# Optimization experiments

Hardware: AMD Instinct MI355X
Metric: run time of the kernel (lower is better)

## Reference

```python
import jax, jax.numpy as jnp
import numpy as np

B, S, D, H = 2, 2048, 1024, 16
HD = D // H  # 64
SCALE = float(np.sqrt(HD))


def setup_inputs() -> dict:
    key = jax.random.key(0)
    ks = jax.random.split(key, 11)
    def lin(kw, kb, fan_in):
        bound = 1.0 / np.sqrt(fan_in)
        W = jax.random.uniform(kw, (D, D), jnp.float32, -bound, bound)
        b = jax.random.uniform(kb, (D,), jnp.float32, -bound, bound)
        return W, b
    Wq, bq = lin(ks[0], ks[1], D)
    Wk, bk = lin(ks[2], ks[3], D)
    Wv, bv = lin(ks[4], ks[5], D)
    Wo, bo = lin(ks[6], ks[7], D)
    q = jax.random.normal(ks[8], (B, S, D), jnp.float32)
    k = jax.random.normal(ks[9], (B, S, D), jnp.float32)
    v = jax.random.normal(ks[10], (B, S, D), jnp.float32)
    mask = jnp.ones((B, 1, S, S), jnp.int32)
    return {"q": q, "k": k, "v": v, "mask": mask,
            "Wq": Wq, "bq": bq, "Wk": Wk, "bk": bk,
            "Wv": Wv, "bv": bv, "Wo": Wo, "bo": bo}


def reference(q, k, v, mask, Wq, bq, Wk, bk, Wv, bv, Wo, bo):
    # torch Linear: x @ W.T + b
    def proj(x, W, b):
        y = x @ W.T + b                      # [B,S,D]
        return y.reshape(B, -1, H, HD).transpose(0, 2, 1, 3)  # [B,H,S,HD]
    Q = proj(q, Wq, bq)
    K = proj(k, Wk, bk)
    V = proj(v, Wv, bv)
    scores = jnp.einsum('bhqd,bhkd->bhqk', Q, K) / SCALE     # [B,H,S,S]
    scores = jnp.where(mask == 0, -1e9, scores)
    attn = jax.nn.softmax(scores, axis=-1)                   # dropout in eval mode = identity
    out = jnp.einsum('bhqk,bhkd->bhqd', attn, V)             # [B,H,S,HD]
    out = out.transpose(0, 2, 1, 3).reshape(B, -1, D)        # [B,S,D]
    return out @ Wo.T + bo
```

## Files before the change

kernel.cpp:

```cpp
#include <hip/hip_runtime.h>
#include <math.h>

#define BB 2
#define SS 2048
#define DD 1024
#define HH 16
#define HDIM 64
#define KK 1024
#define MM 4096
#define KSPLIT 2

#define QFOLD 0.18033688011112042f

typedef _Float16 f16x2 __attribute__((ext_vector_type(2)));
typedef _Float16 f16x4 __attribute__((ext_vector_type(4)));
typedef _Float16 f16x8 __attribute__((ext_vector_type(8)));
typedef float    f32x4 __attribute__((ext_vector_type(4)));

#define GLL16(gp, lp) __builtin_amdgcn_global_load_lds(                        \
    (const __attribute__((address_space(1))) void*)(gp),                       \
    (__attribute__((address_space(3))) void*)(lp), 16, 0, 0)

static __device__ __forceinline__ float fast_exp2(float x) {
    float r;
    asm("v_exp_f32 %0, %1" : "=v"(r) : "v"(x));
    return r;
}
static __device__ __forceinline__ float fast_log2(float x) {
    float r;
    asm("v_log_f32 %0, %1" : "=v"(r) : "v"(x));
    return r;
}
static __device__ __forceinline__ f16x2 cvt_pk(float a, float b) {
    f16x2 r;
    asm("v_cvt_pkrtz_f16_f32 %0, %1, %2" : "=v"(r) : "v"(a), "v"(b));
    return r;
}

__global__ __launch_bounds__(256) void prep(
    const float* __restrict__ q,  const float* __restrict__ k,
    const float* __restrict__ v,  const float* __restrict__ wq,
    const float* __restrict__ wk, const float* __restrict__ wv,
    const float* __restrict__ wo, const int* __restrict__ mask,
    _Float16* __restrict__ qh,  _Float16* __restrict__ kh,
    _Float16* __restrict__ vh,  _Float16* __restrict__ wqh,
    _Float16* __restrict__ wkh, _Float16* __restrict__ wvh,
    _Float16* __restrict__ woh, unsigned short* __restrict__ bm16)
{
    if (blockIdx.x < 16384u) {
        const unsigned u  = blockIdx.x * 256u + threadIdx.x;
        const unsigned U1 = 1u << 20;
        const unsigned U2 = 1u << 18;
        const float* src; _Float16* dst; unsigned off;
        float sc = 1.0f;
        if (u < 3u * U1) {
            const unsigned t = u >> 20; off = u & (U1 - 1u);
            src = (t == 0) ? q  : (t == 1) ? k  : v;
            dst = (t == 0) ? qh : (t == 1) ? kh : vh;
        } else {
            const unsigned r = u - 3u * U1;
            const unsigned t = r >> 18; off = r & (U2 - 1u);
            src = (t == 0) ? wq  : (t == 1) ? wk  : (t == 2) ? wv  : wo;
            dst = (t == 0) ? wqh : (t == 1) ? wkh : (t == 2) ? wvh : woh;
            if (t == 0) sc = QFOLD;
        }
        const float4 x = ((const float4*)src)[off];
        f16x4 y;
        y[0] = (_Float16)(x.x * sc); y[1] = (_Float16)(x.y * sc);
        y[2] = (_Float16)(x.z * sc); y[3] = (_Float16)(x.w * sc);
        ((f16x4*)dst)[off] = y;
    } else {
        const size_t t = (size_t)(blockIdx.x - 16384u) * 256 + threadIdx.x;
        const int4* p = (const int4*)(mask + t * 16);
        const int4 a = p[0], b = p[1], c = p[2], d = p[3];
        unsigned vv = 0;
        vv |= (a.x != 0) << 0;  vv |= (a.y != 0) << 1;
        vv |= (a.z != 0) << 2;  vv |= (a.w != 0) << 3;
        vv |= (b.x != 0) << 4;  vv |= (b.y != 0) << 5;
        vv |= (b.z != 0) << 6;  vv |= (b.w != 0) << 7;
        vv |= (c.x != 0) << 8;  vv |= (c.y != 0) << 9;
        vv |= (c.z != 0) << 10; vv |= (c.w != 0) << 11;
        vv |= (d.x != 0) << 12; vv |= (d.y != 0) << 13;
        vv |= (d.z != 0) << 14; vv |= (d.w != 0) << 15;
        bm16[t] = (unsigned short)vv;
    }
}

#define GEMM_BODY(X, W)                                                        \
    __shared__ _Float16 As[128 * 32];                                          \
    __shared__ _Float16 Bs[64 * 32];                                           \
    const int tid  = threadIdx.x;                                              \
    const int lane = tid & 63;                                                 \
    const int lr   = lane & 15;                                                \
    const int lg   = lane >> 4;                                                \
    const int wave = tid >> 6;                                                 \
    const int wr   = wave >> 1;                                                \
    const int wc   = wave & 1;                                                 \
    const int m0 = blockIdx.y << 7;                                            \
    const int n0 = blockIdx.x << 6;                                            \
    const char* Xb = (const char*)(X);                                         \
    const char* Wb = (const char*)(W);                                         \
    const int pa0 = tid * 16;                                                  \
    const int pa1 = pa0 + 4096;                                                \
    const int ra0 = pa0 >> 6, ca0 = pa0 & 63;                                  \
    const int ra1 = pa1 >> 6, ca1 = pa1 & 63;                                  \
    const int rb0 = pa0 >> 6, cb0 = pa0 & 63;                                  \
    f32x4 acc[4][2] = {};                                                      \
    for (int k0 = 0; k0 < KK; k0 += 32) {                                      \
        GLL16(Xb + ((size_t)(m0 + ra0) * KK + k0) * 2 + ca0, (char*)As + pa0); \
        GLL16(Xb + ((size_t)(m0 + ra1) * KK + k0) * 2 + ca1, (char*)As + pa1); \
        GLL16(Wb + ((size_t)(n0 + rb0) * KK + k0) * 2 + cb0, (char*)Bs + pa0); \
        __syncthreads();                                                       \
        f16x8 af[4], bf[2];                                                    \
        _Pragma("unroll")                                                      \
        for (int mi = 0; mi < 4; ++mi)                                         \
            af[mi] = *(const f16x8*)((const char*)As +                         \
                       ((wr * 64 + mi * 16 + lr) * 64 + lg * 16));             \
        _Pragma("unroll")                                                      \
        for (int ni = 0; ni < 2; ++ni)                                         \
            bf[ni] = *(const f16x8*)((const char*)Bs +                         \
                       ((wc * 32 + ni * 16 + lr) * 64 + lg * 16));             \
        _Pragma("unroll")                                                      \
        for (int mi = 0; mi < 4; ++mi)                                         \
            _Pragma("unroll")                                                  \
            for (int ni = 0; ni < 2; ++ni)                                     \
                acc[mi][ni] = __builtin_amdgcn_mfma_f32_16x16x32_f16(          \
                    af[mi], bf[ni], acc[mi][ni], 0, 0, 0);                     \
        __syncthreads();                                                       \
    }

__global__ __launch_bounds__(256) void gemm_qkv(
    const _Float16* __restrict__ qx, const _Float16* __restrict__ kx,
    const _Float16* __restrict__ vx,
    const _Float16* __restrict__ wqh, const _Float16* __restrict__ wkh,
    const _Float16* __restrict__ wvh,
    const float* __restrict__ bq, const float* __restrict__ bk,
    const float* __restrict__ bv,
    _Float16* __restrict__ Qh, _Float16* __restrict__ Kh,
    _Float16* __restrict__ Vt)
{
    const int z = blockIdx.z;
    const _Float16* X = (z == 0) ? qx : (z == 1) ? kx : vx;
    const _Float16* W = (z == 0) ? wqh : (z == 1) ? wkh : wvh;
    const float* bias = (z == 0) ? bq : (z == 1) ? bk : bv;
    const float bsc   = (z == 0) ? QFOLD : 1.0f;
    _Float16* Yh      = (z == 0) ? Qh : Kh;

    GEMM_BODY(X, W)

    #pragma unroll
    for (int ni = 0; ni < 2; ++ni) {
        const int n  = n0 + wc * 32 + ni * 16 + lr;
        const float bv_ = bias[n] * bsc;
        #pragma unroll
        for (int mi = 0; mi < 4; ++mi) {
            const int mbase = m0 + wr * 64 + mi * 16 + lg * 4;
            if (z < 2) {
                #pragma unroll
                for (int r = 0; r < 4; ++r) {
                    const int m = mbase + r;
                    const int b_ = m >> 11, s_ = m & (SS - 1);
                    const int h_ = n >> 6,  d_ = n & (HDIM - 1);
                    Yh[(((size_t)(b_ * HH + h_)) * SS + s_) * HDIM + d_] =
                        (_Float16)(acc[mi][ni][r] + bv_);
                }
            } else {
                const int b_ = mbase >> 11, s_ = mbase & (SS - 1);
                const int h_ = n >> 6,      d_ = n & (HDIM - 1);
                f16x4 tv;
                #pragma unroll
                for (int r = 0; r < 4; ++r) tv[r] = (_Float16)(acc[mi][ni][r] + bv_);
                *(f16x4*)(Vt + (((size_t)(b_ * HH + h_)) * HDIM + d_) * SS + s_) = tv;
            }
        }
    }
}

__global__ __launch_bounds__(256) void gemm_out(
    const _Float16* __restrict__ X, const _Float16* __restrict__ W,
    const float* __restrict__ bias, float* __restrict__ Y)
{
    GEMM_BODY(X, W)

    #pragma unroll
    for (int ni = 0; ni < 2; ++ni) {
        const int n  = n0 + wc * 32 + ni * 16 + lr;
        const float bv_ = bias[n];
        #pragma unroll
        for (int mi = 0; mi < 4; ++mi) {
            const int mbase = m0 + wr * 64 + mi * 16 + lg * 4;
            #pragma unroll
            for (int r = 0; r < 4; ++r)
                Y[(size_t)(mbase + r) * DD + n] = acc[mi][ni][r] + bv_;
        }
    }
}

__global__ __launch_bounds__(256) void attn_mfma5(
    const _Float16* __restrict__ Qh, const _Float16* __restrict__ Kh,
    const _Float16* __restrict__ Vt, const unsigned long long* __restrict__ bm,
    _Float16* __restrict__ Opart, float* __restrict__ Lpart)
{
    __shared__ _Float16 KbufS[2][4096];
    __shared__ _Float16 VbufS[2][4096];

    const int tid  = threadIdx.x;
    const int lane = tid & 63;
    const int wq   = tid >> 6;
    const int bh   = blockIdx.x;
    const int b_   = bh >> 4;
    const int q0   = blockIdx.y << 7;
    const int ks   = blockIdx.z;
    const int lr   = lane & 15;
    const int lg   = lane >> 4;

    const int NT = SS / 64 / KSPLIT;
    const int t0 = ks * NT;

    const int qrowA = q0 + wq * 32 + lr;
    const int qrowB = qrowA + 16;
    const _Float16* qbA = Qh + ((size_t)bh * SS + qrowA) * HDIM;
    const _Float16* qbB = Qh + ((size_t)bh * SS + qrowB) * HDIM;
    const f16x8 qfA0 = *(const f16x8*)(qbA + lg * 8);
    const f16x8 qfA1 = *(const f16x8*)(qbA + 32 + lg * 8);
    const f16x8 qfB0 = *(const f16x8*)(qbB + lg * 8);
    const f16x8 qfB1 = *(const f16x8*)(qbB + 32 + lg * 8);

    const int c0 = tid, c1 = tid + 256;
    const int kr0 = c0 >> 3, krc0 = (c0 & 7) ^ (kr0 & 7);
    const int kr1 = c1 >> 3, krc1 = (c1 & 7) ^ (kr1 & 7);
    const _Float16* gK0 = Kh + ((size_t)bh * SS + kr0) * HDIM + krc0 * 8;
    const _Float16* gK1 = Kh + ((size_t)bh * SS + kr1) * HDIM + krc1 * 8;
    const _Float16* gV0 = Vt + ((size_t)bh * HDIM + kr0) * SS + krc0 * 8;
    const _Float16* gV1 = Vt + ((size_t)bh * HDIM + kr1) * SS + krc1 * 8;
    const int woff = (tid >> 6) << 10;

    float mA = -INFINITY, mB = -INFINITY;
    f32x4 oaccA[4], oaccB[4];
    #pragma unroll
    for (int dc = 0; dc < 4; ++dc) {
        oaccA[dc] = (f32x4){0.f, 0.f, 0.f, 0.f};
        oaccB[dc] = (f32x4){0.f, 0.f, 0.f, 0.f};
    }
    f32x4 laccA = (f32x4){0.f, 0.f, 0.f, 0.f};
    f32x4 laccB = (f32x4){0.f, 0.f, 0.f, 0.f};

    f16x8 ones;
    #pragma unroll
    for (int e = 0; e < 8; ++e) ones[e] = (_Float16)1.0f;

    const unsigned long long* bmrowA = bm + ((size_t)b_ * SS + qrowA) * (SS / 64);
    const unsigned long long* bmrowB = bm + ((size_t)b_ * SS + qrowB) * (SS / 64);

#define STAGE(KT, BSEL) do {                                                   \
    GLL16(gK0 + (size_t)(KT) * HDIM, (char*)KbufS[BSEL] + woff);               \
    GLL16(gK1 + (size_t)(KT) * HDIM, (char*)KbufS[BSEL] + 4096 + woff);        \
    GLL16(gV0 + (KT), (char*)VbufS[BSEL] + woff);                              \
    GLL16(gV1 + (KT), (char*)VbufS[BSEL] + 4096 + woff);                       \
  } while (0)

    STAGE(t0 * 64, 0);
    __syncthreads();

    const int xk0 = ((lg       ^ (lr & 7)) << 4);
    const int xk1 = (((4 + lg) ^ (lr & 7)) << 4);
    const int xv  = ((lr & 7) << 4);

    unsigned long long bmA = bmrowA[t0];
    unsigned long long bmB = bmrowB[t0];

    for (int ti = 0; ti < NT; ++ti) {
        const int t = t0 + ti;
        const int cur = ti & 1;
        if (ti < NT - 1) STAGE((t + 1) * 64, cur ^ 1);
        unsigned long long bmA_n = 0, bmB_n = 0;
        if (ti < NT - 1) { bmA_n = bmrowA[t + 1]; bmB_n = bmrowB[t + 1]; }

        const char* kb = (const char*)KbufS[cur];
        const char* vb = (const char*)VbufS[cur];

        f32x4 sA[4], sB[4];
        __builtin_amdgcn_s_setprio(1);
        #pragma unroll
        for (int kg = 0; kg < 4; ++kg) {
            const char* rp = kb + (kg * 16 + lr) * 128;
            const f16x8 kf0 = *(const f16x8*)(rp + xk0);
            const f16x8 kf1 = *(const f16x8*)(rp + xk1);
            f32x4 a = (f32x4){0.f, 0.f, 0.f, 0.f};
            a = __builtin_amdgcn_mfma_f32_16x16x32_f16(kf0, qfA0, a, 0, 0, 0);
            a = __builtin_amdgcn_mfma_f32_16x16x32_f16(kf1, qfA1, a, 0, 0, 0);
            sA[kg] = a;
            f32x4 b2 = (f32x4){0.f, 0.f, 0.f, 0.f};
            b2 = __builtin_amdgcn_mfma_f32_16x16x32_f16(kf0, qfB0, b2, 0, 0, 0);
            b2 = __builtin_amdgcn_mfma_f32_16x16x32_f16(kf1, qfB1, b2, 0, 0, 0);
            sB[kg] = b2;
        }
        __builtin_amdgcn_s_setprio(0);

        float svA[16], svB[16];
        #pragma unroll
        for (int kg = 0; kg < 4; ++kg)
            #pragma unroll
            for (int r = 0; r < 4; ++r) {
                svA[kg * 4 + r] = sA[kg][r];
                svB[kg * 4 + r] = sB[kg][r];
            }

        if (~bmA) {
            #pragma unroll
            for (int kg = 0; kg < 4; ++kg)
                #pragma unroll
                for (int r = 0; r < 4; ++r)
                    if (!((bmA >> (kg * 16 + lg * 4 + r)) & 1ull))
                        svA[kg * 4 + r] = -1e9f;
        }
        if (~bmB) {
            #pragma unroll
            for (int kg = 0; kg < 4; ++kg)
                #pragma unroll
                for (int r = 0; r < 4; ++r)
                    if (!((bmB >> (kg * 16 + lg * 4 + r)) & 1ull))
                        svB[kg * 4 + r] = -1e9f;
        }
        bmA = bmA_n; bmB = bmB_n;

        float pmA = svA[0], pmB = svB[0];
        #pragma unroll
        for (int i = 1; i < 16; ++i) {
            pmA = fmaxf(pmA, svA[i]);
            pmB = fmaxf(pmB, svB[i]);
        }
        pmA = fmaxf(pmA, __shfl_xor(pmA, 16));
        pmA = fmaxf(pmA, __shfl_xor(pmA, 32));
        pmB = fmaxf(pmB, __shfl_xor(pmB, 16));
        pmB = fmaxf(pmB, __shfl_xor(pmB, 32));

        if (!__all(pmA <= mA + 8.0f)) {
            const float m_new = fmaxf(mA, pmA);
            const float corr  = fast_exp2(mA - m_new);
            #pragma unroll
            for (int dc = 0; dc < 4; ++dc) oaccA[dc] *= corr;
            laccA *= corr;
            mA = m_new;
        }
        if (!__all(pmB <= mB + 8.0f)) {
            const float m_new = fmaxf(mB, pmB);
            const float corr  = fast_exp2(mB - m_new);
            #pragma unroll
            for (int dc = 0; dc < 4; ++dc) oaccB[dc] *= corr;
            laccB *= corr;
            mB = m_new;
        }

        float pA[16], pB[16];
        #pragma unroll
        for (int i = 0; i < 16; ++i) {
            pA[i] = fast_exp2(svA[i] - mA);
            pB[i] = fast_exp2(svB[i] - mB);
        }

        union { f16x2 h2[4]; f16x8 v8; } uA0, uA1, uB0, uB1;
        #pragma unroll
        for (int e = 0; e < 4; ++e) {
            uA0.h2[e] = cvt_pk(pA[2 * e],     pA[2 * e + 1]);
            uA1.h2[e] = cvt_pk(pA[8 + 2 * e], pA[9 + 2 * e]);
            uB0.h2[e] = cvt_pk(pB[2 * e],     pB[2 * e + 1]);
            uB1.h2[e] = cvt_pk(pB[8 + 2 * e], pB[9 + 2 * e]);
        }
        const f16x8 pbA0 = uA0.v8, pbA1 = uA1.v8;
        const f16x8 pbB0 = uB0.v8, pbB1 = uB1.v8;

        __builtin_amdgcn_s_setprio(1);
        #pragma unroll
        for (int dc = 0; dc < 4; ++dc) {
            const char* rp = vb + (dc * 16 + lr) * 128;
            const f16x4 a0 = *(const f16x4*)(rp + ((0  + lg * 8) ^ xv));
            const f16x4 a1 = *(const f16x4*)(rp + ((32 + lg * 8) ^ xv));
            const f16x4 a2 = *(const f16x4*)(rp + ((64 + lg * 8) ^ xv));
            const f16x4 a3 = *(const f16x4*)(rp + ((96 + lg * 8) ^ xv));
            const f16x8 va0 = __builtin_shufflevector(a0, a1, 0, 1, 2, 3, 4, 5, 6, 7);
            const f16x8 va1 = __builtin_shufflevector(a2, a3, 0, 1, 2, 3, 4, 5, 6, 7);
            oaccA[dc] = __builtin_amdgcn_mfma_f32_16x16x32_f16(va0, pbA0, oaccA[dc], 0, 0, 0);
            oaccA[dc] = __builtin_amdgcn_mfma_f32_16x16x32_f16(va1, pbA1, oaccA[dc], 0, 0, 0);
            oaccB[dc] = __builtin_amdgcn_mfma_f32_16x16x32_f16(va0, pbB0, oaccB[dc], 0, 0, 0);
            oaccB[dc] = __builtin_amdgcn_mfma_f32_16x16x32_f16(va1, pbB1, oaccB[dc], 0, 0, 0);
        }
        laccA = __builtin_amdgcn_mfma_f32_16x16x32_f16(ones, pbA0, laccA, 0, 0, 0);
        laccA = __builtin_amdgcn_mfma_f32_16x16x32_f16(ones, pbA1, laccA, 0, 0, 0);
        laccB = __builtin_amdgcn_mfma_f32_16x16x32_f16(ones, pbB0, laccB, 0, 0, 0);
        laccB = __builtin_amdgcn_mfma_f32_16x16x32_f16(ones, pbB1, laccB, 0, 0, 0);
        __builtin_amdgcn_s_setprio(0);
        __syncthreads();
    }
#undef STAGE

    _Float16* Op = Opart + (size_t)ks * (BB * HH) * SS * HDIM;
    float*    Lp = Lpart + (size_t)ks * (BB * HH) * SS;

    const float invlA = 1.0f / laccA[0];
    const float invlB = 1.0f / laccB[0];
    const float LA_ = mA + fast_log2(laccA[0]);
    const float LB_ = mB + fast_log2(laccB[0]);

    _Float16* opA = Op + ((size_t)bh * SS + qrowA) * HDIM;
    _Float16* opB = Op + ((size_t)bh * SS + qrowB) * HDIM;
    #pragma unroll
    for (int dc = 0; dc < 4; ++dc) {
        f16x4 rA, rB;
        #pragma unroll
        for (int r = 0; r < 4; ++r) {
            rA[r] = (_Float16)(oaccA[dc][r] * invlA);
            rB[r] = (_Float16)(oaccB[dc][r] * invlB);
        }
        *reinterpret_cast<f16x4*>(opA + dc * 16 + lg * 4) = rA;
        *reinterpret_cast<f16x4*>(opB + dc * 16 + lg * 4) = rB;
    }
    if (lg == 0) {
        Lp[(size_t)bh * SS + qrowA] = LA_;
        Lp[(size_t)bh * SS + qrowB] = LB_;
    }
}

__global__ __launch_bounds__(256) void combine(
    const _Float16* __restrict__ Opart, const float* __restrict__ Lpart,
    _Float16* __restrict__ AO)
{
    const int tid = threadIdx.x;
    const int row = blockIdx.x * 32 + (tid >> 3);
    const int dc  = (tid & 7) * 8;
    const int bh = row >> 11, s = row & (SS - 1);
    const int b_ = bh >> 4,   h_ = bh & (HH - 1);
    const size_t PER = (size_t)(BB * HH) * SS;

    const float L0 = Lpart[row], L1 = Lpart[PER + row];
    const float Ls = fmaxf(L0, L1);
    const float w0 = fast_exp2(L0 - Ls);
    const float w1 = fast_exp2(L1 - Ls);
    const float inv = 1.0f / (w0 + w1);

    const f16x8 a = *(const f16x8*)(Opart + (size_t)row * HDIM + dc);
    const f16x8 b = *(const f16x8*)(Opart + PER * HDIM + (size_t)row * HDIM + dc);
    f16x8 r;
    #pragma unroll
    for (int i = 0; i < 8; ++i)
        r[i] = (_Float16)(((float)a[i] * w0 + (float)b[i] * w1) * inv);
    *(f16x8*)(AO + ((size_t)b_ * SS + s) * DD + h_ * HDIM + dc) = r;
}

extern "C" void kernel_launch(void* const* d_in, const int* in_sizes, int n_in,
                              void* d_out, int out_size, void* d_ws, size_t ws_size,
                              hipStream_t stream)
{
    const float* q    = (const float*)d_in[0];
    const float* k    = (const float*)d_in[1];
    const float* v    = (const float*)d_in[2];
    const int*   mask = (const int*)d_in[3];
    const float* Wq   = (const float*)d_in[4];
    const float* bq   = (const float*)d_in[5];
    const float* Wk   = (const float*)d_in[6];
    const float* bk   = (const float*)d_in[7];
    const float* Wv   = (const float*)d_in[8];
    const float* bv   = (const float*)d_in[9];
    const float* Wo   = (const float*)d_in[10];
    const float* bo   = (const float*)d_in[11];
    float* out = (float*)d_out;

    char* w = (char*)d_ws;
    _Float16* qx  = (_Float16*)(w);
    _Float16* kx  = (_Float16*)(w + 8  * 1048576);
    _Float16* vx  = (_Float16*)(w + 16 * 1048576);
    _Float16* wqh = (_Float16*)(w + 24 * 1048576);
    _Float16* wkh = (_Float16*)(w + 26 * 1048576);
    _Float16* wvh = (_Float16*)(w + 28 * 1048576);
    _Float16* woh = (_Float16*)(w + 30 * 1048576);
    _Float16* Qh  = (_Float16*)(w + 32 * 1048576);
    _Float16* Kh  = (_Float16*)(w + 40 * 1048576);
    _Float16* Vt  = (_Float16*)(w + 48 * 1048576);
    unsigned long long* bm = (unsigned long long*)(w + 56 * 1048576);
    _Float16* Opart = (_Float16*)(w + 8 * 1048576);
    float*    Lpart = (float*)(w + 24 * 1048576);
    _Float16* AO    = (_Float16*)(w);

    prep<<<18432, 256, 0, stream>>>(q, k, v, Wq, Wk, Wv, Wo, mask,
                                    qx, kx, vx, wqh, wkh, wvh, woh,
                                    (unsigned short*)bm);

    const dim3 gqkv(DD / 64, MM / 128, 3);
    gemm_qkv<<<gqkv, 256, 0, stream>>>(qx, kx, vx, wqh, wkh, wvh,
                                       bq, bk, bv, Qh, Kh, Vt);

    const dim3 gattn(BB * HH, SS / 128, KSPLIT);
    attn_mfma5<<<gattn, 256, 0, stream>>>(Qh, Kh, Vt, bm, Opart, Lpart);

    combine<<<2048, 256, 0, stream>>>(Opart, Lpart, AO);

    const dim3 gout(DD / 64, MM / 128);
    gemm_out<<<gout, 256, 0, stream>>>(AO, woh, bo, out);
}
```

Measured before the change: 175.5 us.

## Load K/V fragments directly from global memory instead of staging through LDS

The attention kernel drops the double-buffered LDS staging of K and V tiles (global_load_lds plus per-iteration barriers). Each wave now reads its MFMA operand fragments straight from global memory, relying on L1/L2 for reuse across the four waves of a block. This removes LDS traffic and the __syncthreads per tile. The cost is redundant global loads across waves, no explicit prefetch of the next tile, and small 8-byte strided reads for V that may expose memory latency.

```diff
diff --git a/kernel.cpp b/kernel.cpp
--- a/kernel.cpp
+++ b/kernel.cpp
@@ -196,14 +196,11 @@
     }
 }
 
-__global__ __launch_bounds__(256) void attn_mfma5(
+__global__ __launch_bounds__(256) void attn_mfma6(
     const _Float16* __restrict__ Qh, const _Float16* __restrict__ Kh,
     const _Float16* __restrict__ Vt, const unsigned long long* __restrict__ bm,
     _Float16* __restrict__ Opart, float* __restrict__ Lpart)
 {
-    __shared__ _Float16 KbufS[2][4096];
-    __shared__ _Float16 VbufS[2][4096];
-
     const int tid  = threadIdx.x;
     const int lane = tid & 63;
     const int wq   = tid >> 6;
@@ -226,14 +223,8 @@
     const f16x8 qfB0 = *(const f16x8*)(qbB + lg * 8);
     const f16x8 qfB1 = *(const f16x8*)(qbB + 32 + lg * 8);
 
-    const int c0 = tid, c1 = tid + 256;
-    const int kr0 = c0 >> 3, krc0 = (c0 & 7) ^ (kr0 & 7);
-    const int kr1 = c1 >> 3, krc1 = (c1 & 7) ^ (kr1 & 7);
-    const _Float16* gK0 = Kh + ((size_t)bh * SS + kr0) * HDIM + krc0 * 8;
-    const _Float16* gK1 = Kh + ((size_t)bh * SS + kr1) * HDIM + krc1 * 8;
-    const _Float16* gV0 = Vt + ((size_t)bh * HDIM + kr0) * SS + krc0 * 8;
-    const _Float16* gV1 = Vt + ((size_t)bh * HDIM + kr1) * SS + krc1 * 8;
-    const int woff = (tid >> 6) << 10;
+    const _Float16* Kg = Kh + (size_t)bh * SS * HDIM + (size_t)lr * HDIM + lg * 8;
+    const _Float16* Vg = Vt + (size_t)bh * HDIM * SS + (size_t)lr * SS + lg * 4;
 
     float mA = -INFINITY, mB = -INFINITY;
     f32x4 oaccA[4], oaccB[4];
@@ -252,40 +243,22 @@
     const unsigned long long* bmrowA = bm + ((size_t)b_ * SS + qrowA) * (SS / 64);
     const unsigned long long* bmrowB = bm + ((size_t)b_ * SS + qrowB) * (SS / 64);
 
-#define STAGE(KT, BSEL) do {                                                   \
-    GLL16(gK0 + (size_t)(KT) * HDIM, (char*)KbufS[BSEL] + woff);               \
-    GLL16(gK1 + (size_t)(KT) * HDIM, (char*)KbufS[BSEL] + 4096 + woff);        \
-    GLL16(gV0 + (KT), (char*)VbufS[BSEL] + woff);                              \
-    GLL16(gV1 + (KT), (char*)VbufS[BSEL] + 4096 + woff);                       \
-  } while (0)
-
-    STAGE(t0 * 64, 0);
-    __syncthreads();
-
-    const int xk0 = ((lg       ^ (lr & 7)) << 4);
-    const int xk1 = (((4 + lg) ^ (lr & 7)) << 4);
-    const int xv  = ((lr & 7) << 4);
-
     unsigned long long bmA = bmrowA[t0];
     unsigned long long bmB = bmrowB[t0];
 
     for (int ti = 0; ti < NT; ++ti) {
-        const int t = t0 + ti;
-        const int cur = ti & 1;
-        if (ti < NT - 1) STAGE((t + 1) * 64, cur ^ 1);
+        const int t  = t0 + ti;
+        const int kt = t * 64;
         unsigned long long bmA_n = 0, bmB_n = 0;
         if (ti < NT - 1) { bmA_n = bmrowA[t + 1]; bmB_n = bmrowB[t + 1]; }
 
-        const char* kb = (const char*)KbufS[cur];
-        const char* vb = (const char*)VbufS[cur];
-
         f32x4 sA[4], sB[4];
         __builtin_amdgcn_s_setprio(1);
         #pragma unroll
         for (int kg = 0; kg < 4; ++kg) {
-            const char* rp = kb + (kg * 16 + lr) * 128;
-            const f16x8 kf0 = *(const f16x8*)(rp + xk0);
-            const f16x8 kf1 = *(const f16x8*)(rp + xk1);
+            const _Float16* kp = Kg + (size_t)(kt + kg * 16) * HDIM;
+            const f16x8 kf0 = *(const f16x8*)(kp);
+            const f16x8 kf1 = *(const f16x8*)(kp + 32);
             f32x4 a = (f32x4){0.f, 0.f, 0.f, 0.f};
             a = __builtin_amdgcn_mfma_f32_16x16x32_f16(kf0, qfA0, a, 0, 0, 0);
             a = __builtin_amdgcn_mfma_f32_16x16x32_f16(kf1, qfA1, a, 0, 0, 0);
@@ -373,11 +346,11 @@
         __builtin_amdgcn_s_setprio(1);
         #pragma unroll
         for (int dc = 0; dc < 4; ++dc) {
-            const char* rp = vb + (dc * 16 + lr) * 128;
-            const f16x4 a0 = *(const f16x4*)(rp + ((0  + lg * 8) ^ xv));
-            const f16x4 a1 = *(const f16x4*)(rp + ((32 + lg * 8) ^ xv));
-            const f16x4 a2 = *(const f16x4*)(rp + ((64 + lg * 8) ^ xv));
-            const f16x4 a3 = *(const f16x4*)(rp + ((96 + lg * 8) ^ xv));
+            const _Float16* vp = Vg + (size_t)(dc * 16) * SS + kt;
+            const f16x4 a0 = *(const f16x4*)(vp);
+            const f16x4 a1 = *(const f16x4*)(vp + 16);
+            const f16x4 a2 = *(const f16x4*)(vp + 32);
+            const f16x4 a3 = *(const f16x4*)(vp + 48);
             const f16x8 va0 = __builtin_shufflevector(a0, a1, 0, 1, 2, 3, 4, 5, 6, 7);
             const f16x8 va1 = __builtin_shufflevector(a2, a3, 0, 1, 2, 3, 4, 5, 6, 7);
             oaccA[dc] = __builtin_amdgcn_mfma_f32_16x16x32_f16(va0, pbA0, oaccA[dc], 0, 0, 0);
@@ -390,9 +363,7 @@
         laccB = __builtin_amdgcn_mfma_f32_16x16x32_f16(ones, pbB0, laccB, 0, 0, 0);
         laccB = __builtin_amdgcn_mfma_f32_16x16x32_f16(ones, pbB1, laccB, 0, 0, 0);
         __builtin_amdgcn_s_setprio(0);
-        __syncthreads();
-    }
-#undef STAGE
+    }
 
     _Float16* Op = Opart + (size_t)ks * (BB * HH) * SS * HDIM;
     float*    Lp = Lpart + (size_t)ks * (BB * HH) * SS;
@@ -490,7 +461,7 @@
                                        bq, bk, bv, Qh, Kh, Vt);
 
     const dim3 gattn(BB * HH, SS / 128, KSPLIT);
-    attn_mfma5<<<gattn, 256, 0, stream>>>(Qh, Kh, Vt, bm, Opart, Lpart);
+    attn_mfma6<<<gattn, 256, 0, stream>>>(Qh, Kh, Vt, bm, Opart, Lpart);
 
     combine<<<2048, 256, 0, stream>>>(Opart, Lpart, AO);
 
```

After: 306.7 us. 1.75x slower.
